# Kernel tuning notes

Measured on AMD Instinct MI355X. Metric: run time of the kernel, lower is better.

## Reference

```python
import jax, jax.numpy as jnp
import numpy as np

N_EMB = 2048
EMB_DIM = 512
EPS_IN = 1e-5  # instance-norm epsilon (torch default used in instance_norm)


def setup_inputs() -> dict:
    key = jax.random.key(0)
    kx, ke = jax.random.split(key)
    x = jax.random.normal(kx, (32, 1024, EMB_DIM), dtype=jnp.float32)
    # codebook init: uniform(-1/M, 1/M), then row-normalized (as in __init__)
    init_bound = 1.0 / N_EMB
    emb = jax.random.uniform(ke, (N_EMB, EMB_DIM), dtype=jnp.float32,
                             minval=-init_bound, maxval=init_bound)
    emb = emb / (jnp.linalg.norm(emb, axis=1, keepdims=True) + 1e-4)
    return {"x": x, "embedding": emb}


def _instance_norm(x, axis, eps=EPS_IN):
    mu = jnp.mean(x, axis=axis, keepdims=True)
    # torch.std default is unbiased (ddof=1)
    std = jnp.std(x, axis=axis, keepdims=True, ddof=1)
    return (x - mu) / (std + eps)


def reference(x, embedding):
    N, T, D = x.shape
    M = embedding.shape[0]
    z = _instance_norm(x, axis=1)  # normalize over time dim

    # normalized codebook only used for distance computation
    emb_n = embedding / (jnp.linalg.norm(embedding, axis=1, keepdims=True) + 1e-4)

    z_flat = jax.lax.stop_gradient(z).reshape(-1, D)  # (N*T, D)
    # ||e||^2 + ||z||^2 - 2 z.e  (addmm with alpha=-2, beta=1)
    distances = (jnp.sum(emb_n ** 2, axis=1)[None, :]
                 + jnp.sum(z_flat ** 2, axis=1, keepdims=True)
                 - 2.0 * (z_flat @ emb_n.T))  # (N*T, M)
    indices = jnp.argmin(distances.astype(jnp.float32), axis=-1)  # (N*T,)

    # lookup uses the UN-normalized embedding buffer (as in original)
    quantized = embedding[indices].reshape(N, T, D)

    commitment_loss = jnp.mean((z - jax.lax.stop_gradient(quantized)) ** 2)

    quantized_ste = z + jax.lax.stop_gradient(quantized - z)
    quantized_out = (quantized_ste + quantized) / 2.0

    # avg_probs = mean of one-hot encodings == normalized histogram
    counts = jnp.zeros((M,), dtype=jnp.float32).at[indices].add(1.0)
    avg_probs = counts / z_flat.shape[0]
    perplexity = jnp.exp(-jnp.sum(avg_probs * jnp.log(avg_probs + 1e-10)))

    return quantized_out, commitment_loss, perplexity
```

## Files before the change

### kernel.cpp

```cpp
#include <hip/hip_runtime.h>

#define T_DIM 1024
#define D_DIM 512
#define M_CODES 2048
#define NT 32768
#define TOTAL 16777216

typedef float f32x4 __attribute__((ext_vector_type(4)));
typedef unsigned int u32;
typedef unsigned long long u64;

#define WS_MU    0
#define WS_S     65536
#define WS_CE    131072
#define WS_KEYS  139264
#define WS_EB    401408
#define WS_HIST  (401408 + 1048576)
#define WS_LPART (WS_HIST + 8192)

__device__ __forceinline__ void gload16(const void* g, void* l) {
    __builtin_amdgcn_global_load_lds(
        (const __attribute__((address_space(1))) u32*)g,
        (__attribute__((address_space(3))) u32*)l, 16, 0, 0);
}

__device__ __forceinline__ float block_reduce_sum_256(float v) {
    #pragma unroll
    for (int s = 32; s; s >>= 1) v += __shfl_xor(v, s, 64);
    __shared__ float ls[4];
    int w = threadIdx.x >> 6;
    if ((threadIdx.x & 63) == 0) ls[w] = v;
    __syncthreads();
    float r = (ls[0] + ls[1]) + (ls[2] + ls[3]);
    __syncthreads();
    return r;
}

__device__ __forceinline__ u32 pk_fp8x4(float a, float b, float c, float d) {
    u32 w = __builtin_amdgcn_cvt_pk_fp8_f32(a, b, 0, false);
    w = __builtin_amdgcn_cvt_pk_fp8_f32(c, d, w, true);
    return w;
}

__device__ __forceinline__ u32 mono(float f) {
    u32 u = __float_as_uint(f);
    return u ^ (0x80000000u | (u32)((int)u >> 31));
}

__device__ __forceinline__ int pk_dest(int d, int row) {
    return (d & ~31) | ((((d >> 3) & 3) ^ ((row >> 2) & 3)) << 3) | (d & 7);
}

__global__ void stats_kernel(const float* __restrict__ x,
                             float* __restrict__ mu_o, float* __restrict__ s_o) {
    int n = blockIdx.y;
    int lane = threadIdx.x & 63;
    int d = blockIdx.x * 64 + lane;
    int tg = threadIdx.x >> 6;
    const float* xp = x + (size_t)n * (T_DIM * D_DIM) + d;
    float sum = 0.f, sq = 0.f;
    int t0 = tg * 256;
    for (int it = 0; it < 256; ++it) {
        float v = xp[(size_t)(t0 + it) * D_DIM];
        sum += v; sq += v * v;
    }
    __shared__ float ssum[4][64], ssq[4][64];
    ssum[tg][lane] = sum;
    ssq[tg][lane] = sq;
    __syncthreads();
    if (threadIdx.x < 64) {
        int l = threadIdx.x;
        float s1 = (ssum[0][l] + ssum[1][l]) + (ssum[2][l] + ssum[3][l]);
        float q1 = (ssq[0][l] + ssq[1][l]) + (ssq[2][l] + ssq[3][l]);
        float mu = s1 * (1.0f / 1024.0f);
        float var = (q1 - 1024.0f * mu * mu) * (1.0f / 1023.0f);
        var = fmaxf(var, 0.0f);
        float sd = sqrtf(var) + 1e-5f;
        int nd = n * D_DIM + blockIdx.x * 64 + l;
        mu_o[nd] = mu; s_o[nd] = sd;
    }
}

__global__ void codebook_kernel(const float* __restrict__ emb,
                                unsigned char* __restrict__ eb, float* __restrict__ ce) {
    int j = blockIdx.x;
    int d = threadIdx.x * 2;
    float2 e = *(const float2*)&emb[(size_t)j * D_DIM + d];
    float sq = e.x * e.x + e.y * e.y;
    float norm2 = block_reduce_sum_256(sq);
    float den = sqrtf(norm2) + 1e-4f;
    float en0 = e.x / den, en1 = e.y / den;
    u32 w = __builtin_amdgcn_cvt_pk_fp8_f32(en0, en1, 0, false);
    *(unsigned short*)&eb[(size_t)j * D_DIM + pk_dest(d, j)] =
        (unsigned short)(w & 0xFFFF);
    float cep = en0 * en0 + en1 * en1;
    float cesum = block_reduce_sum_256(cep);
    if (threadIdx.x == 0) ce[j] = cesum;
}

__global__ void pack_kernel(const float* __restrict__ x, const float* __restrict__ mu,
                            const float* __restrict__ s, unsigned char* __restrict__ zq) {
    int i = blockIdx.x * 4 + (threadIdx.x >> 6);
    int lane = threadIdx.x & 63;
    int n = i >> 10;
    const float* xp = x + (size_t)i * D_DIM;
    const float* mp = mu + n * D_DIM;
    const float* sp = s + n * D_DIM;
    #pragma unroll
    for (int c = 0; c < 2; ++c) {
        int d = c * 256 + lane * 4;
        float4 xv = *(const float4*)&xp[d];
        float4 mv = *(const float4*)&mp[d];
        float4 sv = *(const float4*)&sp[d];
        float z0 = (xv.x - mv.x) / sv.x;
        float z1 = (xv.y - mv.y) / sv.y;
        float z2 = (xv.z - mv.z) / sv.z;
        float z3 = (xv.w - mv.w) / sv.w;
        *(u32*)&zq[(size_t)i * D_DIM + pk_dest(d, i)] = pk_fp8x4(z0, z1, z2, z3);
    }
}

__global__ __launch_bounds__(512, 2) void gemm_argmin(
    const unsigned char* __restrict__ zq, const unsigned char* __restrict__ eb,
    const float* __restrict__ ce, u64* __restrict__ keys) {
    __shared__ long smem[4][2048];
    int tid = threadIdx.x;
    int bid = blockIdx.x;
    int swz = (bid & 7) * 128 + (bid >> 3);
    int n0 = (swz & 7) * 256;
    int m0 = (swz >> 3) * 256;

    f32x4 acc[4][8];
    #pragma unroll
    for (int a = 0; a < 4; ++a)
        #pragma unroll
        for (int b = 0; b < 8; ++b) acc[a][b] = (f32x4)0.0f;

    int w = tid >> 6, l = tid & 63;
    int wm = (w >> 1) * 64;
    int wn = (w & 1) * 128;
    int fr = l & 15, fg = l >> 4;
    int xfg = fg ^ ((fr >> 2) & 3);

    int rS = 32 * w + (l >> 1);
    int hS = (l & 1) * 16;
    size_t srcA = (size_t)(m0 + rS) * D_DIM + hS;
    size_t srcB = (size_t)(n0 + rS) * D_DIM + hS;

    #define STAGE(buf, t) do {                                                    \
        gload16(zq + srcA + (t) * 32, &smem[buf][w * 128]);                       \
        gload16(eb + srcB + (t) * 32, &smem[buf][1024 + w * 128]);                \
    } while (0)

    STAGE(0, 0);
    STAGE(1, 1);
    STAGE(2, 2);
    asm volatile("s_waitcnt vmcnt(4)" ::: "memory");
    __builtin_amdgcn_s_barrier();
    __builtin_amdgcn_sched_barrier(0);

    for (int t = 0; t < 16; ++t) {
        int cur = t & 3;
        if (t <= 12) STAGE((t + 3) & 3, t + 3);
        long av[4], bv[8];
        #pragma unroll
        for (int i = 0; i < 4; ++i)
            av[i] = smem[cur][(wm + i * 16 + fr) * 4 + xfg];
        #pragma unroll
        for (int j = 0; j < 8; ++j)
            bv[j] = smem[cur][1024 + (wn + j * 16 + fr) * 4 + xfg];
        __builtin_amdgcn_s_setprio(1);
        #pragma unroll
        for (int mb = 0; mb < 4; ++mb)
            #pragma unroll
            for (int nb = 0; nb < 8; ++nb)
                acc[mb][nb] = __builtin_amdgcn_mfma_f32_16x16x32_fp8_fp8(
                    av[mb], bv[nb], acc[mb][nb], 0, 0, 0);
        __builtin_amdgcn_s_setprio(0);
        if (t < 15) {
            if (t <= 12)      asm volatile("s_waitcnt vmcnt(4)" ::: "memory");
            else if (t == 13) asm volatile("s_waitcnt vmcnt(2)" ::: "memory");
            else              asm volatile("s_waitcnt vmcnt(0)" ::: "memory");
            __builtin_amdgcn_s_barrier();
            __builtin_amdgcn_sched_barrier(0);
        }
    }
    #undef STAGE

    #pragma unroll
    for (int mb = 0; mb < 4; ++mb) {
        #pragma unroll
        for (int r = 0; r < 4; ++r) {
            int q = m0 + wm + mb * 16 + fg * 4 + r;
            u64 best = ~0ULL;
            #pragma unroll
            for (int nb = 0; nb < 8; ++nb) {
                int j = n0 + wn + nb * 16 + fr;
                float dist = ce[j] - 2.0f * acc[mb][nb][r];
                u64 key = ((u64)mono(dist) << 32) | (unsigned)j;
                if (key < best) best = key;
            }
            #pragma unroll
            for (int sft = 1; sft < 16; sft <<= 1) {
                u64 o = __shfl_xor(best, sft, 64);
                if (o < best) best = o;
            }
            if (fr == 0) atomicMin(keys + q, best);
        }
    }
}

__global__ void output_kernel(const float* __restrict__ x, const float* __restrict__ mu,
                              const float* __restrict__ s, const float* __restrict__ emb,
                              const u64* __restrict__ keys,
                              float* __restrict__ out, float* __restrict__ loss_part,
                              unsigned* __restrict__ hist) {
    int i = blockIdx.x * 4 + (threadIdx.x >> 6);
    int lane = threadIdx.x & 63;
    int n = i >> 10;
    unsigned idx = (unsigned)(keys[i] & 0xFFFFFFFFULL);
    float lsum = 0.f;
    #pragma unroll
    for (int c = 0; c < 2; ++c) {
        int d = c * 256 + lane * 4;
        float4 xv = *(const float4*)&x[(size_t)i * D_DIM + d];
        float4 mv = *(const float4*)&mu[n * D_DIM + d];
        float4 sv = *(const float4*)&s[n * D_DIM + d];
        float4 ev = *(const float4*)&emb[(size_t)idx * D_DIM + d];
        float z0 = (xv.x - mv.x) / sv.x;
        float z1 = (xv.y - mv.y) / sv.y;
        float z2 = (xv.z - mv.z) / sv.z;
        float z3 = (xv.w - mv.w) / sv.w;
        float o0 = ((z0 + (ev.x - z0)) + ev.x) * 0.5f;
        float o1 = ((z1 + (ev.y - z1)) + ev.y) * 0.5f;
        float o2 = ((z2 + (ev.z - z2)) + ev.z) * 0.5f;
        float o3 = ((z3 + (ev.w - z3)) + ev.w) * 0.5f;
        *(float4*)&out[(size_t)i * D_DIM + d] = make_float4(o0, o1, o2, o3);
        lsum += (z0 - ev.x) * (z0 - ev.x) + (z1 - ev.y) * (z1 - ev.y)
              + (z2 - ev.z) * (z2 - ev.z) + (z3 - ev.w) * (z3 - ev.w);
    }
    #pragma unroll
    for (int sft = 32; sft; sft >>= 1) lsum += __shfl_xor(lsum, sft, 64);
    __shared__ float ls[4];
    if (lane == 0) {
        ls[threadIdx.x >> 6] = lsum;
        atomicAdd(&hist[idx], 1u);
    }
    __syncthreads();
    if (threadIdx.x == 0)
        loss_part[blockIdx.x] = (ls[0] + ls[1]) + (ls[2] + ls[3]);
}

__global__ void final_kernel(const unsigned* __restrict__ hist,
                             const float* __restrict__ loss_part, float* __restrict__ out) {
    float h = 0.f;
    for (int b = threadIdx.x; b < M_CODES; b += 256) {
        float p = (float)hist[b] * (1.0f / 32768.0f);
        h += p * logf(p + 1e-10f);
    }
    h = block_reduce_sum_256(h);
    float lsum = 0.f;
    for (int b = threadIdx.x; b < NT / 4; b += 256) lsum += loss_part[b];
    lsum = block_reduce_sum_256(lsum);
    if (threadIdx.x == 0) {
        out[TOTAL] = lsum * (1.0f / 16777216.0f);
        out[TOTAL + 1] = expf(-h);
    }
}

extern "C" void kernel_launch(void* const* d_in, const int* in_sizes, int n_in,
                              void* d_out, int out_size, void* d_ws, size_t ws_size,
                              hipStream_t stream) {
    (void)in_sizes; (void)n_in; (void)out_size; (void)ws_size;
    const float* x = (const float*)d_in[0];
    const float* emb = (const float*)d_in[1];
    float* out = (float*)d_out;
    char* ws = (char*)d_ws;
    float* mu   = (float*)(ws + WS_MU);
    float* s    = (float*)(ws + WS_S);
    float* ce   = (float*)(ws + WS_CE);
    u64* keys = (u64*)(ws + WS_KEYS);
    unsigned char* eb = (unsigned char*)(ws + WS_EB);
    unsigned* hist = (unsigned*)(ws + WS_HIST);
    float* loss_part = (float*)(ws + WS_LPART);
    unsigned char* zq = (unsigned char*)d_out;

    (void)hipMemsetAsync(ws + WS_KEYS, 0xFF, 262144, stream);
    (void)hipMemsetAsync(ws + WS_HIST, 0x00, 8192, stream);

    stats_kernel<<<dim3(8, 32), 256, 0, stream>>>(x, mu, s);
    codebook_kernel<<<M_CODES, 256, 0, stream>>>(emb, eb, ce);
    pack_kernel<<<NT / 4, 256, 0, stream>>>(x, mu, s, zq);
    gemm_argmin<<<1024, 512, 0, stream>>>(zq, eb, ce, keys);
    output_kernel<<<NT / 4, 256, 0, stream>>>(x, mu, s, emb, keys, out, loss_part, hist);
    final_kernel<<<1, 256, 0, stream>>>(hist, loss_part, out);
}
```

Measured before the change: 163.4 us.

## Fuse fp8 packing into stats kernel and cut GEMM LDS ring to three stages

Merges pack_kernel into the stats kernel, so each block re-reads its 64-column slice of x right after computing mean and std and writes the fp8-packed normalized rows, removing one kernel launch. Separately, the GEMM's LDS pipeline goes from four buffers with prefetch distance three to three buffers with distance two, which cuts shared memory use but leaves less latency hiding. The fused pack runs on only 256 blocks with strided 16-byte reads and 4-byte scattered writes, so it may have worse parallelism and coalescing than the old 8192-block pack kernel.

```diff
diff --git a/kernel.cpp b/kernel.cpp
--- a/kernel.cpp
+++ b/kernel.cpp
@@ -51,8 +51,9 @@
     return (d & ~31) | ((((d >> 3) & 3) ^ ((row >> 2) & 3)) << 3) | (d & 7);
 }
 
-__global__ void stats_kernel(const float* __restrict__ x,
-                             float* __restrict__ mu_o, float* __restrict__ s_o) {
+__global__ void prep_kernel(const float* __restrict__ x,
+                            float* __restrict__ mu_o, float* __restrict__ s_o,
+                            unsigned char* __restrict__ zq) {
     int n = blockIdx.y;
     int lane = threadIdx.x & 63;
     int d = blockIdx.x * 64 + lane;
@@ -65,6 +66,7 @@
         sum += v; sq += v * v;
     }
     __shared__ float ssum[4][64], ssq[4][64];
+    __shared__ float smu[64], ssd[64];
     ssum[tg][lane] = sum;
     ssq[tg][lane] = sq;
     __syncthreads();
@@ -78,6 +80,24 @@
         float sd = sqrtf(var) + 1e-5f;
         int nd = n * D_DIM + blockIdx.x * 64 + l;
         mu_o[nd] = mu; s_o[nd] = sd;
+        smu[l] = mu; ssd[l] = sd;
+    }
+    __syncthreads();
+    int q = threadIdx.x & 15;
+    int tg2 = threadIdx.x >> 4;
+    int dq = q * 4;
+    float4 muv = *(const float4*)&smu[dq];
+    float4 sdv = *(const float4*)&ssd[dq];
+    int dglob = blockIdx.x * 64 + dq;
+    for (int tt = 0; tt < 64; ++tt) {
+        int t = tg2 * 64 + tt;
+        float4 xv = *(const float4*)&x[((size_t)n * T_DIM + t) * D_DIM + dglob];
+        float z0 = (xv.x - muv.x) / sdv.x;
+        float z1 = (xv.y - muv.y) / sdv.y;
+        float z2 = (xv.z - muv.z) / sdv.z;
+        float z3 = (xv.w - muv.w) / sdv.w;
+        int i = (n << 10) + t;
+        *(u32*)&zq[(size_t)i * D_DIM + pk_dest(dglob, i)] = pk_fp8x4(z0, z1, z2, z3);
     }
 }
 
@@ -98,32 +118,10 @@
     if (threadIdx.x == 0) ce[j] = cesum;
 }
 
-__global__ void pack_kernel(const float* __restrict__ x, const float* __restrict__ mu,
-                            const float* __restrict__ s, unsigned char* __restrict__ zq) {
-    int i = blockIdx.x * 4 + (threadIdx.x >> 6);
-    int lane = threadIdx.x & 63;
-    int n = i >> 10;
-    const float* xp = x + (size_t)i * D_DIM;
-    const float* mp = mu + n * D_DIM;
-    const float* sp = s + n * D_DIM;
-    #pragma unroll
-    for (int c = 0; c < 2; ++c) {
-        int d = c * 256 + lane * 4;
-        float4 xv = *(const float4*)&xp[d];
-        float4 mv = *(const float4*)&mp[d];
-        float4 sv = *(const float4*)&sp[d];
-        float z0 = (xv.x - mv.x) / sv.x;
-        float z1 = (xv.y - mv.y) / sv.y;
-        float z2 = (xv.z - mv.z) / sv.z;
-        float z3 = (xv.w - mv.w) / sv.w;
-        *(u32*)&zq[(size_t)i * D_DIM + pk_dest(d, i)] = pk_fp8x4(z0, z1, z2, z3);
-    }
-}
-
 __global__ __launch_bounds__(512, 2) void gemm_argmin(
     const unsigned char* __restrict__ zq, const unsigned char* __restrict__ eb,
     const float* __restrict__ ce, u64* __restrict__ keys) {
-    __shared__ long smem[4][2048];
+    __shared__ long smem[3][2048];
     int tid = threadIdx.x;
     int bid = blockIdx.x;
     int swz = (bid & 7) * 128 + (bid >> 3);
@@ -154,21 +152,20 @@
 
     STAGE(0, 0);
     STAGE(1, 1);
-    STAGE(2, 2);
-    asm volatile("s_waitcnt vmcnt(4)" ::: "memory");
+    asm volatile("s_waitcnt vmcnt(2)" ::: "memory");
     __builtin_amdgcn_s_barrier();
     __builtin_amdgcn_sched_barrier(0);
 
+    int rd = 0, wr = 2;
     for (int t = 0; t < 16; ++t) {
-        int cur = t & 3;
-        if (t <= 12) STAGE((t + 3) & 3, t + 3);
+        if (t <= 13) STAGE(wr, t + 2);
         long av[4], bv[8];
         #pragma unroll
         for (int i = 0; i < 4; ++i)
-            av[i] = smem[cur][(wm + i * 16 + fr) * 4 + xfg];
+            av[i] = smem[rd][(wm + i * 16 + fr) * 4 + xfg];
         #pragma unroll
         for (int j = 0; j < 8; ++j)
-            bv[j] = smem[cur][1024 + (wn + j * 16 + fr) * 4 + xfg];
+            bv[j] = smem[rd][1024 + (wn + j * 16 + fr) * 4 + xfg];
         __builtin_amdgcn_s_setprio(1);
         #pragma unroll
         for (int mb = 0; mb < 4; ++mb)
@@ -178,12 +175,13 @@
                     av[mb], bv[nb], acc[mb][nb], 0, 0, 0);
         __builtin_amdgcn_s_setprio(0);
         if (t < 15) {
-            if (t <= 12)      asm volatile("s_waitcnt vmcnt(4)" ::: "memory");
-            else if (t == 13) asm volatile("s_waitcnt vmcnt(2)" ::: "memory");
-            else              asm volatile("s_waitcnt vmcnt(0)" ::: "memory");
+            if (t <= 13) asm volatile("s_waitcnt vmcnt(2)" ::: "memory");
+            else         asm volatile("s_waitcnt vmcnt(0)" ::: "memory");
             __builtin_amdgcn_s_barrier();
             __builtin_amdgcn_sched_barrier(0);
         }
+        if (++rd == 3) rd = 0;
+        if (++wr == 3) wr = 0;
     }
     #undef STAGE
 
@@ -288,9 +286,8 @@
     (void)hipMemsetAsync(ws + WS_KEYS, 0xFF, 262144, stream);
     (void)hipMemsetAsync(ws + WS_HIST, 0x00, 8192, stream);
 
-    stats_kernel<<<dim3(8, 32), 256, 0, stream>>>(x, mu, s);
+    prep_kernel<<<dim3(8, 32), 256, 0, stream>>>(x, mu, s, zq);
     codebook_kernel<<<M_CODES, 256, 0, stream>>>(emb, eb, ce);
-    pack_kernel<<<NT / 4, 256, 0, stream>>>(x, mu, s, zq);
     gemm_argmin<<<1024, 512, 0, stream>>>(zq, eb, ce, keys);
     output_kernel<<<NT / 4, 256, 0, stream>>>(x, mu, s, emb, keys, out, loss_part, hist);
     final_kernel<<<1, 256, 0, stream>>>(hist, loss_part, out);
```

Result: slower. 175.2 us (+7.2%).

## Keep codebook tile resident in LDS and stream activations into registers

Applied to the files above, without the earlier changes.

The GEMM-argmin kernel now loads its full 256-code fp8 codebook slice (all 512 dims) into LDS once. Each of 256 persistent blocks then loops over four 256-row activation tiles. Activation fragments are read straight from global memory into registers with a two-stage register prefetch, and the pack kernel writes plain unswizzled rows to match. This removes the per-k-step LDS staging and barriers for A and the repeated B reloads. In exchange, the large LDS footprint limits occupancy to one block per CU, and A global-load latency is covered only by a shallow prefetch, with duplicate A reads across wave pairs.

```diff
diff --git a/kernel.cpp b/kernel.cpp
--- a/kernel.cpp
+++ b/kernel.cpp
@@ -116,25 +116,20 @@
         float z1 = (xv.y - mv.y) / sv.y;
         float z2 = (xv.z - mv.z) / sv.z;
         float z3 = (xv.w - mv.w) / sv.w;
-        *(u32*)&zq[(size_t)i * D_DIM + pk_dest(d, i)] = pk_fp8x4(z0, z1, z2, z3);
+        *(u32*)&zq[(size_t)i * D_DIM + d] = pk_fp8x4(z0, z1, z2, z3);
     }
 }
 
 __global__ __launch_bounds__(512, 2) void gemm_argmin(
     const unsigned char* __restrict__ zq, const unsigned char* __restrict__ eb,
     const float* __restrict__ ce, u64* __restrict__ keys) {
-    __shared__ long smem[4][2048];
+    __shared__ long bsm[16384];
     int tid = threadIdx.x;
     int bid = blockIdx.x;
-    int swz = (bid & 7) * 128 + (bid >> 3);
-    int n0 = (swz & 7) * 256;
-    int m0 = (swz >> 3) * 256;
-
-    f32x4 acc[4][8];
-    #pragma unroll
-    for (int a = 0; a < 4; ++a)
-        #pragma unroll
-        for (int b = 0; b < 8; ++b) acc[a][b] = (f32x4)0.0f;
+    int x = bid & 7;
+    int q = bid >> 3;
+    int n0 = (q & 7) * 256;
+    int mc = x * 4 + (q >> 3);
 
     int w = tid >> 6, l = tid & 63;
     int wm = (w >> 1) * 64;
@@ -142,70 +137,78 @@
     int fr = l & 15, fg = l >> 4;
     int xfg = fg ^ ((fr >> 2) & 3);
 
-    int rS = 32 * w + (l >> 1);
-    int hS = (l & 1) * 16;
-    size_t srcA = (size_t)(m0 + rS) * D_DIM + hS;
-    size_t srcB = (size_t)(n0 + rS) * D_DIM + hS;
-
-    #define STAGE(buf, t) do {                                                    \
-        gload16(zq + srcA + (t) * 32, &smem[buf][w * 128]);                       \
-        gload16(eb + srcB + (t) * 32, &smem[buf][1024 + w * 128]);                \
-    } while (0)
-
-    STAGE(0, 0);
-    STAGE(1, 1);
-    STAGE(2, 2);
-    asm volatile("s_waitcnt vmcnt(4)" ::: "memory");
-    __builtin_amdgcn_s_barrier();
-    __builtin_amdgcn_sched_barrier(0);
-
-    for (int t = 0; t < 16; ++t) {
-        int cur = t & 3;
-        if (t <= 12) STAGE((t + 3) & 3, t + 3);
-        long av[4], bv[8];
-        #pragma unroll
-        for (int i = 0; i < 4; ++i)
-            av[i] = smem[cur][(wm + i * 16 + fr) * 4 + xfg];
+    #pragma unroll
+    for (int k = 0; k < 16; ++k)
+        gload16(eb + (size_t)(n0 + 32 * w + 2 * k) * D_DIM + l * 16,
+                &bsm[(32 * w + 2 * k) * 64]);
+    __syncthreads();
+
+    #pragma unroll 1
+    for (int mt = 0; mt < 4; ++mt) {
+        int m0 = mc * 1024 + mt * 256;
+        f32x4 acc[4][8];
+        #pragma unroll
+        for (int a = 0; a < 4; ++a)
+            #pragma unroll
+            for (int b = 0; b < 8; ++b) acc[a][b] = (f32x4)0.0f;
+
+        const unsigned char* abase[4];
+        long abuf[2][4];
+        #pragma unroll
+        for (int i = 0; i < 4; ++i) {
+            abase[i] = zq + (size_t)(m0 + wm + i * 16 + fr) * D_DIM + fg * 8;
+            abuf[0][i] = *(const long*)(abase[i]);
+            abuf[1][i] = *(const long*)(abase[i] + 32);
+        }
+        long bbuf[2][8];
         #pragma unroll
         for (int j = 0; j < 8; ++j)
-            bv[j] = smem[cur][1024 + (wn + j * 16 + fr) * 4 + xfg];
-        __builtin_amdgcn_s_setprio(1);
-        #pragma unroll
-        for (int mb = 0; mb < 4; ++mb)
+            bbuf[0][j] = bsm[(wn + j * 16 + fr) * 64 + xfg];
+
+        #pragma unroll
+        for (int t = 0; t < 16; ++t) {
+            int cs = t & 1, ns = cs ^ 1;
+            if (t < 15) {
+                #pragma unroll
+                for (int j = 0; j < 8; ++j)
+                    bbuf[ns][j] = bsm[(wn + j * 16 + fr) * 64 + (t + 1) * 4 + xfg];
+            }
+            long av[4];
             #pragma unroll
-            for (int nb = 0; nb < 8; ++nb)
-                acc[mb][nb] = __builtin_amdgcn_mfma_f32_16x16x32_fp8_fp8(
-                    av[mb], bv[nb], acc[mb][nb], 0, 0, 0);
-        __builtin_amdgcn_s_setprio(0);
-        if (t < 15) {
-            if (t <= 12)      asm volatile("s_waitcnt vmcnt(4)" ::: "memory");
-            else if (t == 13) asm volatile("s_waitcnt vmcnt(2)" ::: "memory");
-            else              asm volatile("s_waitcnt vmcnt(0)" ::: "memory");
-            __builtin_amdgcn_s_barrier();
-            __builtin_amdgcn_sched_barrier(0);
-        }
-    }
-    #undef STAGE
-
-    #pragma unroll
-    for (int mb = 0; mb < 4; ++mb) {
-        #pragma unroll
-        for (int r = 0; r < 4; ++r) {
-            int q = m0 + wm + mb * 16 + fg * 4 + r;
-            u64 best = ~0ULL;
-            #pragma unroll
-            for (int nb = 0; nb < 8; ++nb) {
-                int j = n0 + wn + nb * 16 + fr;
-                float dist = ce[j] - 2.0f * acc[mb][nb][r];
-                u64 key = ((u64)mono(dist) << 32) | (unsigned)j;
-                if (key < best) best = key;
+            for (int i = 0; i < 4; ++i) av[i] = abuf[cs][i];
+            if (t < 14) {
+                #pragma unroll
+                for (int i = 0; i < 4; ++i)
+                    abuf[cs][i] = *(const long*)(abase[i] + (t + 2) * 32);
             }
             #pragma unroll
-            for (int sft = 1; sft < 16; sft <<= 1) {
-                u64 o = __shfl_xor(best, sft, 64);
-                if (o < best) best = o;
+            for (int mb = 0; mb < 4; ++mb)
+                #pragma unroll
+                for (int nb = 0; nb < 8; ++nb)
+                    acc[mb][nb] = __builtin_amdgcn_mfma_f32_16x16x32_fp8_fp8(
+                        av[mb], bbuf[cs][nb], acc[mb][nb], 0, 0, 0);
+        }
+
+        #pragma unroll
+        for (int mb = 0; mb < 4; ++mb) {
+            #pragma unroll
+            for (int r = 0; r < 4; ++r) {
+                int qrow = m0 + wm + mb * 16 + fg * 4 + r;
+                u64 best = ~0ULL;
+                #pragma unroll
+                for (int nb = 0; nb < 8; ++nb) {
+                    int j = n0 + wn + nb * 16 + fr;
+                    float dist = ce[j] - 2.0f * acc[mb][nb][r];
+                    u64 key = ((u64)mono(dist) << 32) | (unsigned)j;
+                    if (key < best) best = key;
+                }
+                #pragma unroll
+                for (int sft = 1; sft < 16; sft <<= 1) {
+                    u64 o = __shfl_xor(best, sft, 64);
+                    if (o < best) best = o;
+                }
+                if (fr == 0) atomicMin(keys + qrow, best);
             }
-            if (fr == 0) atomicMin(keys + q, best);
         }
     }
 }
@@ -291,7 +294,7 @@
     stats_kernel<<<dim3(8, 32), 256, 0, stream>>>(x, mu, s);
     codebook_kernel<<<M_CODES, 256, 0, stream>>>(emb, eb, ce);
     pack_kernel<<<NT / 4, 256, 0, stream>>>(x, mu, s, zq);
-    gemm_argmin<<<1024, 512, 0, stream>>>(zq, eb, ce, keys);
+    gemm_argmin<<<256, 512, 0, stream>>>(zq, eb, ce, keys);
     output_kernel<<<NT / 4, 256, 0, stream>>>(x, mu, s, emb, keys, out, loss_part, hist);
     final_kernel<<<1, 256, 0, stream>>>(hist, loss_part, out);
 }
```

New measurement: 250.0 us. 1.53x slower.
